# Kernel optimization log

Measured on AMD Instinct MI355X. Metric: run time of the kernel, lower is better.

Reference implementation:

```python
import jax, jax.numpy as jnp
import numpy as np

CLIP_MEAN = np.array([0.48145466, 0.4578275, 0.40821073], dtype=np.float32)
CLIP_STD = np.array([0.26862954, 0.26130258, 0.27577711], dtype=np.float32)


def setup_inputs() -> dict:
    key = jax.random.key(0)
    k_img, k_x, k_y, k_w, k_h = jax.random.split(key, 5)
    C, H, W = 3, 2048, 2048
    N = 256
    MAXB, MINB = 320, 32  # bbox side range in pixels
    img = jax.random.uniform(k_img, (C, H, W), dtype=jnp.float32, minval=0.0, maxval=255.0)
    x0 = jax.random.randint(k_x, (N,), 0, W - MAXB)
    y0 = jax.random.randint(k_y, (N,), 0, H - MAXB)
    bw = jax.random.randint(k_w, (N,), MINB, MAXB)
    bh = jax.random.randint(k_h, (N,), MINB, MAXB)
    bboxes = jnp.stack([x0, y0, x0 + bw, y0 + bh], axis=1).astype(jnp.int32)  # [N,4] xyxy
    return {
        "img": img,
        "mean": jnp.asarray(CLIP_MEAN),
        "std": jnp.asarray(CLIP_STD),
        "bboxes": bboxes,
        "size": 224,
    }


def _crop_resize(img, bboxes, size):
    """Batched crop-to-bbox + short-edge resize + center-crop == sample the
    central square (side = min(bh, bw)) of each bbox onto a size x size grid
    with bilinear interpolation. img: [C,H,W] float, bboxes: [N,4] int xyxy.
    Returns [N,C,size,size]."""
    C, H, W = img.shape
    b = bboxes.astype(jnp.float32)
    x0, y0, x1, y1 = b[:, 0], b[:, 1], b[:, 2], b[:, 3]
    side = jnp.minimum(x1 - x0, y1 - y0)            # [N]
    cx, cy = (x0 + x1) * 0.5, (y0 + y1) * 0.5        # [N]
    # output pixel j -> source coord start + (j+0.5)*scale - 0.5 (torch resize convention)
    grid = (jnp.arange(size, dtype=jnp.float32) + 0.5) / size  # [S]
    sx = (cx - side * 0.5)[:, None] + grid[None, :] * side[:, None] - 0.5  # [N,S]
    sy = (cy - side * 0.5)[:, None] + grid[None, :] * side[:, None] - 0.5  # [N,S]
    sx = jnp.clip(sx, 0.0, W - 1.0)
    sy = jnp.clip(sy, 0.0, H - 1.0)
    ix0 = jnp.floor(sx).astype(jnp.int32)
    iy0 = jnp.floor(sy).astype(jnp.int32)
    ix1 = jnp.minimum(ix0 + 1, W - 1)
    iy1 = jnp.minimum(iy0 + 1, H - 1)
    wx = (sx - ix0.astype(jnp.float32))[None, :, None, :]  # broadcast over C and y
    wy = (sy - iy0.astype(jnp.float32))[None, :, :, None]  # broadcast over C and x
    # gathers -> [C,N,S,S]
    p00 = img[:, iy0[:, :, None], ix0[:, None, :]]
    p01 = img[:, iy0[:, :, None], ix1[:, None, :]]
    p10 = img[:, iy1[:, :, None], ix0[:, None, :]]
    p11 = img[:, iy1[:, :, None], ix1[:, None, :]]
    top = p00 + wx * (p01 - p00)
    bot = p10 + wx * (p11 - p10)
    patches = top + wy * (bot - top)                 # [C,N,S,S]
    return jnp.transpose(patches, (1, 0, 2, 3))      # [N,C,S,S]


def reference(img, mean, std, bboxes, size):
    patches = _crop_resize(img, bboxes, size)        # [N,3,S,S]
    patches = patches / 255.0                        # ToFloat scaling
    return (patches - mean[None, :, None, None]) / std[None, :, None, None]
```

## Files before the change

### kernel.cpp

```cpp
#include <hip/hip_runtime.h>


#define S      224
#define IMG_H  2048
#define IMG_W  2048

__global__ __launch_bounds__(256) void patch_kernel(
    const float* __restrict__ img,
    const float* __restrict__ mean,
    const float* __restrict__ stdd,
    const int*   __restrict__ bboxes,
    float*       __restrict__ out)
{
    const int n   = blockIdx.y;
    const int pix = blockIdx.x * 256 + threadIdx.x;
    const int oy  = pix / S;
    const int ox  = pix - oy * S;

    const float x0 = (float)bboxes[n * 4 + 0];
    const float y0 = (float)bboxes[n * 4 + 1];
    const float x1 = (float)bboxes[n * 4 + 2];
    const float y1 = (float)bboxes[n * 4 + 3];

    const float side  = fminf(x1 - x0, y1 - y0);
    const float basex = (x0 + x1) * 0.5f - side * 0.5f - 0.5f;
    const float basey = (y0 + y1) * 0.5f - side * 0.5f - 0.5f;
    const float invS  = 1.0f / (float)S;

    float sx = fmaf((ox + 0.5f) * invS, side, basex);
    float sy = fmaf((oy + 0.5f) * invS, side, basey);
    sx = fminf(fmaxf(sx, 0.0f), (float)(IMG_W - 1));
    sy = fminf(fmaxf(sy, 0.0f), (float)(IMG_H - 1));

    const int ix0 = (int)floorf(sx);
    const int iy0 = (int)floorf(sy);
    const int ix1 = min(ix0 + 1, IMG_W - 1);
    const int iy1 = min(iy0 + 1, IMG_H - 1);
    const float wx = sx - (float)ix0;
    const float wy = sy - (float)iy0;

    const size_t r0 = (size_t)iy0 * IMG_W;
    const size_t r1 = (size_t)iy1 * IMG_W;

#pragma unroll
    for (int c = 0; c < 3; ++c) {
        const float* __restrict__ p = img + (size_t)c * (IMG_H * IMG_W);
        const float p00 = p[r0 + ix0];
        const float p01 = p[r0 + ix1];
        const float p10 = p[r1 + ix0];
        const float p11 = p[r1 + ix1];
        const float top = fmaf(wx, p01 - p00, p00);
        const float bot = fmaf(wx, p11 - p10, p10);
        const float v   = fmaf(wy, bot - top, top);

        const float m  = mean[c];
        const float sd = stdd[c];
        const float o = fmaf(v, 1.0f / (255.0f * sd), -m / sd);

        out[(((size_t)n * 3 + c) * S + (size_t)oy) * S + ox] = o;
    }
}

extern "C" void kernel_launch(void* const* d_in, const int* in_sizes, int n_in,
                              void* d_out, int out_size, void* d_ws, size_t ws_size,
                              hipStream_t stream)
{
    const float* img    = (const float*)d_in[0];
    const float* mean   = (const float*)d_in[1];
    const float* stdd   = (const float*)d_in[2];
    const int*   bboxes = (const int*)d_in[3];
    float* out = (float*)d_out;

    const int N = in_sizes[3] / 4;
    dim3 grid(S * S / 256, N);
    patch_kernel<<<grid, 256, 0, stream>>>(img, mean, stdd, bboxes, out);
}
```

Before: 232.1 us.

## Stage bilinear source rows in LDS, one block per output row

Each block now handles one output row of one box. It loads the two source rows for all three channels into shared memory with contiguous loads, then does the bilinear interpolation from LDS. This replaces twelve scattered global gathers per output pixel with coalesced row loads plus LDS reads. The cost is a block-wide barrier, partly idle threads in the last compute iteration, and an LDS footprint tied to a fixed pitch that assumes box widths stay below a bound.

After: 293.3 us. 1.26x slower.

```diff
diff --git a/kernel.cpp b/kernel.cpp
--- a/kernel.cpp
+++ b/kernel.cpp
@@ -4,6 +4,7 @@
 #define S      224
 #define IMG_H  2048
 #define IMG_W  2048
+#define PITCH  328
 
 __global__ __launch_bounds__(256) void patch_kernel(
     const float* __restrict__ img,
@@ -12,52 +13,66 @@
     const int*   __restrict__ bboxes,
     float*       __restrict__ out)
 {
-    const int n   = blockIdx.y;
-    const int pix = blockIdx.x * 256 + threadIdx.x;
-    const int oy  = pix / S;
-    const int ox  = pix - oy * S;
+    const int n  = blockIdx.y;
+    const int oy = blockIdx.x;
+    const int tid = threadIdx.x;
+
+    __shared__ float lds[6][PITCH];
 
     const float x0 = (float)bboxes[n * 4 + 0];
     const float y0 = (float)bboxes[n * 4 + 1];
     const float x1 = (float)bboxes[n * 4 + 2];
     const float y1 = (float)bboxes[n * 4 + 3];
-
     const float side  = fminf(x1 - x0, y1 - y0);
     const float basex = (x0 + x1) * 0.5f - side * 0.5f - 0.5f;
     const float basey = (y0 + y1) * 0.5f - side * 0.5f - 0.5f;
     const float invS  = 1.0f / (float)S;
 
-    float sx = fmaf((ox + 0.5f) * invS, side, basex);
     float sy = fmaf((oy + 0.5f) * invS, side, basey);
-    sx = fminf(fmaxf(sx, 0.0f), (float)(IMG_W - 1));
     sy = fminf(fmaxf(sy, 0.0f), (float)(IMG_H - 1));
+    const int   iy0 = (int)floorf(sy);
+    const int   iy1 = min(iy0 + 1, IMG_H - 1);
+    const float wy  = sy - (float)iy0;
 
-    const int ix0 = (int)floorf(sx);
-    const int iy0 = (int)floorf(sy);
-    const int ix1 = min(ix0 + 1, IMG_W - 1);
-    const int iy1 = min(iy0 + 1, IMG_H - 1);
-    const float wx = sx - (float)ix0;
-    const float wy = sy - (float)iy0;
+    float sx_first = fmaf((0   + 0.5f) * invS, side, basex);
+    float sx_last  = fmaf((223 + 0.5f) * invS, side, basex);
+    sx_first = fminf(fmaxf(sx_first, 0.0f), (float)(IMG_W - 1));
+    sx_last  = fminf(fmaxf(sx_last,  0.0f), (float)(IMG_W - 1));
+    const int ix_lo = (int)floorf(sx_first);
+    const int ix_hi = min((int)floorf(sx_last) + 1, IMG_W - 1);
+    const int L     = ix_hi - ix_lo + 1;
 
-    const size_t r0 = (size_t)iy0 * IMG_W;
-    const size_t r1 = (size_t)iy1 * IMG_W;
+    for (int rc = 0; rc < 6; ++rc) {
+        const int r = (rc < 3) ? iy0 : iy1;
+        const int c = (rc < 3) ? rc  : rc - 3;
+        const float* __restrict__ src =
+            img + (size_t)c * (IMG_H * IMG_W) + (size_t)r * IMG_W + ix_lo;
+        for (int off = tid; off < L; off += 256)
+            lds[rc][off] = src[off];
+    }
+    __syncthreads();
 
-#pragma unroll
-    for (int c = 0; c < 3; ++c) {
-        const float* __restrict__ p = img + (size_t)c * (IMG_H * IMG_W);
-        const float p00 = p[r0 + ix0];
-        const float p01 = p[r0 + ix1];
-        const float p10 = p[r1 + ix0];
-        const float p11 = p[r1 + ix1];
+    for (int k = tid; k < 3 * S; k += 256) {
+        const int c  = k / S;
+        const int ox = k - c * S;
+
+        float sx = fmaf((ox + 0.5f) * invS, side, basex);
+        sx = fminf(fmaxf(sx, 0.0f), (float)(IMG_W - 1));
+        const int   ix = (int)floorf(sx);
+        const float wx = sx - (float)ix;
+        const int   o0 = ix - ix_lo;
+
+        const float* row0 = lds[c];
+        const float* row1 = lds[3 + c];
+        const float p00 = row0[o0], p01 = row0[o0 + 1];
+        const float p10 = row1[o0], p11 = row1[o0 + 1];
         const float top = fmaf(wx, p01 - p00, p00);
         const float bot = fmaf(wx, p11 - p10, p10);
         const float v   = fmaf(wy, bot - top, top);
 
-        const float m  = mean[c];
         const float sd = stdd[c];
-        const float o = fmaf(v, 1.0f / (255.0f * sd), -m / sd);
-
-        out[(((size_t)n * 3 + c) * S + (size_t)oy) * S + ox] = o;
+        const float o  = fmaf(v, 1.0f / (255.0f * sd), -mean[c] / sd);
+        out[((size_t)(n * 3 + c) * S + (size_t)oy) * S + ox] = o;
     }
 }
 
@@ -72,6 +87,6 @@
     float* out = (float*)d_out;
 
     const int N = in_sizes[3] / 4;
-    dim3 grid(S * S / 256, N);
+    dim3 grid(S, N);
     patch_kernel<<<grid, 256, 0, stream>>>(img, mean, stdd, bboxes, out);
 }
```
